# Optimization experiments

Measured on AMD Instinct MI355X. Metric: run time of the kernel, lower is better.

The kernel has to match this reference:

```python
import jax, jax.numpy as jnp
import numpy as np

B, N, E = 4, 4096, 65536
FIN, FOUT = 128, 64
ALPHA = 0.2          # LeakyReLU negative slope
NEG = -9e15          # mask value from original code


def setup_inputs() -> dict:
    key = jax.random.key(0)
    k1, k2, k3, k4 = jax.random.split(key, 4)
    h = jax.random.normal(k1, (B, N, FIN), dtype=jnp.float32)
    edge_index = jax.random.randint(k2, (B, 2, E), 0, N, dtype=jnp.int32)
    # Xavier-uniform-like params
    W = jax.random.uniform(k3, (FIN, FOUT), jnp.float32, -1.0, 1.0) * (1.414 * np.sqrt(6.0 / (FIN + FOUT)))
    a = jax.random.uniform(k4, (2 * FOUT, 1), jnp.float32, -1.0, 1.0) * (1.414 * np.sqrt(6.0 / (2 * FOUT + 1)))
    return {"h": h, "edge_index": edge_index, "W": W, "a": a}


def reference(h, edge_index, W, a):
    # Wh: [B, N, FOUT]
    Wh = jnp.einsum('bnf,fo->bno', h, W)
    Wh_flat = Wh.reshape(-1, FOUT)  # [B*N, FOUT]

    # Faithful to original: raw node ids (< N) index the flattened tensor,
    # i.e. edge features are gathered from batch 0's rows.
    src = edge_index[:, 0].reshape(-1)  # [B*E]
    tgt = edge_index[:, 1].reshape(-1)  # [B*E]
    a_input = jnp.concatenate([Wh_flat[src], Wh_flat[tgt]], axis=1)  # [B*E, 2*FOUT]
    e = (a_input @ a)[:, 0]  # [B*E]

    b_idx = jnp.repeat(jnp.arange(B), E)
    e_dense = jnp.zeros((B, N, N), e.dtype).at[b_idx, src, tgt].set(e)
    e_dense = jax.nn.leaky_relu(e_dense, ALPHA)

    attention = jnp.where(e_dense > 0, e_dense, NEG)
    attention = jax.nn.softmax(attention, axis=1)  # softmax over dim=1 as in original
    # dropout p=0.0 -> no-op

    h_prime = jnp.einsum('bmn,bnf->bmf', attention, Wh)  # [B, N, FOUT]
    return jax.nn.elu(h_prime)  # concat=True path
```

## Files before the change

kernel.cpp:

```cpp
#include <hip/hip_runtime.h>
#include <hip/hip_bf16.h>

#define BB 4
#define NN 4096
#define EE 65536
#define FIN 128
#define FOUT 64
#define CAP 64

__global__ __launch_bounds__(256) void phase0_kernel(
        const float* __restrict__ h, const float* __restrict__ W, const float* __restrict__ a,
        float* __restrict__ Wh, int* __restrict__ deg, float* __restrict__ D,
        unsigned* __restrict__ bitmap, float* __restrict__ as_, float* __restrict__ at_,
        float* __restrict__ base) {
    __shared__ union {
        struct { float hs[32][132]; float Ws[64][64]; } wh;
        float Wa[256];
    } smem;
    int tid = threadIdx.x;
    int bid = blockIdx.x;
    if (bid < 512) {
        long row0 = (long)bid * 32;
        for (int i = tid; i < 1024; i += 256) {
            float4 v = ((const float4*)(h + row0 * FIN))[i];
            int r = (i * 4) >> 7, c = (i * 4) & 127;
            *(float4*)&smem.wh.hs[r][c] = v;
        }
        int tx = tid & 15, ty = tid >> 4;
        int c0 = tx * 4, r0 = ty * 2;
        float acc[2][4] = {};
        for (int kk = 0; kk < 128; kk += 64) {
            __syncthreads();
            for (int i = tid; i < 1024; i += 256) {
                float4 v = ((const float4*)(W + kk * FOUT))[i];
                int k = (i * 4) >> 6, c = (i * 4) & 63;
                *(float4*)&smem.wh.Ws[k][c] = v;
            }
            __syncthreads();
#pragma unroll
            for (int k = 0; k < 64; k += 4) {
                float4 w0 = *(const float4*)&smem.wh.Ws[k][c0];
                float4 w1 = *(const float4*)&smem.wh.Ws[k + 1][c0];
                float4 w2 = *(const float4*)&smem.wh.Ws[k + 2][c0];
                float4 w3 = *(const float4*)&smem.wh.Ws[k + 3][c0];
#pragma unroll
                for (int r = 0; r < 2; ++r) {
                    float4 hv = *(const float4*)&smem.wh.hs[r0 + r][kk + k];
                    acc[r][0] += hv.x * w0.x + hv.y * w1.x + hv.z * w2.x + hv.w * w3.x;
                    acc[r][1] += hv.x * w0.y + hv.y * w1.y + hv.z * w2.y + hv.w * w3.y;
                    acc[r][2] += hv.x * w0.z + hv.y * w1.z + hv.z * w2.z + hv.w * w3.z;
                    acc[r][3] += hv.x * w0.w + hv.y * w1.w + hv.z * w2.w + hv.w * w3.w;
                }
            }
        }
#pragma unroll
        for (int r = 0; r < 2; ++r)
            *(float4*)&Wh[(row0 + r0 + r) * FOUT + c0] = *(float4*)&acc[r][0];
    } else {
        int local = bid - 512;
        uint4* bm4 = (uint4*)(bitmap + (long)local * 4096);
        for (int i = tid; i < 1024; i += 256) bm4[i] = make_uint4(0u, 0u, 0u, 0u);
        int gid2 = local * 256 + tid;
        if (gid2 < BB * NN) { deg[gid2] = 0; D[gid2] = 0.f; }
        if (gid2 < BB * FOUT) base[gid2] = 0.f;
        {
            int half = tid >> 7, k = tid & 127;
            const float* wr = W + k * FOUT;
            const float* av = a + half * FOUT;
            float s = 0.f;
#pragma unroll
            for (int f2 = 0; f2 < FOUT; ++f2) s += wr[f2] * av[f2];
            smem.Wa[half * 128 + k] = s;
        }
        __syncthreads();
        int lane = tid & 63, wv = tid >> 6;
#pragma unroll
        for (int r = 0; r < 2; ++r) {
            int n = local * 8 + wv * 2 + r;
            float h0v = h[(long)n * FIN + lane];
            float h1v = h[(long)n * FIN + 64 + lane];
            float ps = h0v * smem.Wa[lane] + h1v * smem.Wa[64 + lane];
            float pt = h0v * smem.Wa[128 + lane] + h1v * smem.Wa[192 + lane];
            for (int off = 32; off; off >>= 1) {
                ps += __shfl_down(ps, off);
                pt += __shfl_down(pt, off);
            }
            if (lane == 0) { as_[n] = ps; at_[n] = pt; }
        }
    }
}

__global__ void edge_kernel(const int* __restrict__ ei, const float* __restrict__ as_,
                            const float* __restrict__ at_, unsigned* __restrict__ bitmap,
                            int* __restrict__ deg, int* __restrict__ csr,
                            float* __restrict__ D) {
    int idx = blockIdx.x * 256 + threadIdx.x;
    int b = idx >> 16;
    int j = idx & 65535;
    const int* eb = ei + (long)b * 2 * EE;
    int s = eb[j], t = eb[EE + j];
    float as_s = as_[s];
    if (as_s + at_[t] > 0.f) {
        int row = (b << 12) | s;
        long bit = ((long)row << 12) | t;
        unsigned m = 1u << (bit & 31);
        unsigned old = atomicOr(&bitmap[bit >> 5], m);
        if (!(old & m)) {
            atomicAdd(&D[(b << 12) | t], expf(as_s));
            int slot = atomicAdd(&deg[row], 1);
            if (slot < CAP) csr[row * CAP + slot] = t;
        }
    }
}

__global__ __launch_bounds__(256) void base_kernel(
        const float* __restrict__ D, const float* __restrict__ Wh,
        float* __restrict__ base) {
    __shared__ float part[4][64];
    int tid = threadIdx.x, lane = tid & 63, wv = tid >> 6;
    int bid = blockIdx.x;
    int b = bid >> 4, chunk = bid & 15;
    const float* Db = D + (b << 12);
    const float* Whb = Wh + (((long)b << 12) * FOUT);
    int t0 = chunk * 256 + wv * 64;
    float dv = Db[t0 + lane];
    unsigned long long zmask = __ballot(dv == 0.f);
    float bacc = 0.f;
    while (zmask) {
        int k = __ffsll(zmask) - 1;
        zmask &= zmask - 1;
        bacc += Whb[(t0 + k) * FOUT + lane];
    }
    part[wv][lane] = bacc;
    __syncthreads();
    if (wv == 0) {
        float s = part[0][lane] + part[1][lane] + part[2][lane] + part[3][lane];
        atomicAdd(&base[(b << 6) | lane], s * (1.0f / NN));
    }
}

__global__ __launch_bounds__(256) void gather_kernel(
        const int* __restrict__ deg, const int* __restrict__ csr,
        const float* __restrict__ as_, const float* __restrict__ D,
        const float* __restrict__ Wh, const float* __restrict__ base,
        float* __restrict__ out) {
    int tid = threadIdx.x;
    int lane = tid & 63, wv = tid >> 6;
    int bid = blockIdx.x;
    int b = bid >> 8;
    const float* Db = D + (b << 12);
    const float* Whb = Wh + (((long)b << 12) * FOUT);
    float bsv = base[(b << 6) | lane];

    int row0 = bid * 16 + wv * 4;
    int d0 = min(deg[row0], CAP), d1 = min(deg[row0 + 1], CAP);
    int d2 = min(deg[row0 + 2], CAP), d3 = min(deg[row0 + 3], CAP);
    float E0 = expf(as_[row0 & 4095]), E1 = expf(as_[(row0 + 1) & 4095]);
    float E2 = expf(as_[(row0 + 2) & 4095]), E3 = expf(as_[(row0 + 3) & 4095]);
    const int* c0p = csr + (long)row0 * CAP;
    const int* c1p = c0p + CAP;
    const int* c2p = c1p + CAP;
    const int* c3p = c2p + CAP;
    float a0 = 0.f, a1 = 0.f, a2 = 0.f, a3 = 0.f;
    int dmax = max(max(d0, d1), max(d2, d3));
    for (int j = 0; j < dmax; ++j) {
        if (j < d0) { int t = c0p[j]; a0 += (E0 / Db[t]) * Whb[t * FOUT + lane]; }
        if (j < d1) { int t = c1p[j]; a1 += (E1 / Db[t]) * Whb[t * FOUT + lane]; }
        if (j < d2) { int t = c2p[j]; a2 += (E2 / Db[t]) * Whb[t * FOUT + lane]; }
        if (j < d3) { int t = c3p[j]; a3 += (E3 / Db[t]) * Whb[t * FOUT + lane]; }
    }
    float x0 = a0 + bsv, x1 = a1 + bsv, x2 = a2 + bsv, x3 = a3 + bsv;
    out[(long)row0 * FOUT + lane] = x0 > 0.f ? x0 : expm1f(x0);
    out[(long)(row0 + 1) * FOUT + lane] = x1 > 0.f ? x1 : expm1f(x1);
    out[(long)(row0 + 2) * FOUT + lane] = x2 > 0.f ? x2 : expm1f(x2);
    out[(long)(row0 + 3) * FOUT + lane] = x3 > 0.f ? x3 : expm1f(x3);
}

extern "C" void kernel_launch(void* const* d_in, const int* in_sizes, int n_in,
                              void* d_out, int out_size, void* d_ws, size_t ws_size,
                              hipStream_t stream) {
    const float* h  = (const float*)d_in[0];
    const int*   ei = (const int*)d_in[1];
    const float* W  = (const float*)d_in[2];
    const float* a  = (const float*)d_in[3];
    float* out = (float*)d_out;

    char* ws = (char*)d_ws;
    float*    Wh     = (float*)(ws);
    int*      csr    = (int*)(ws + 4194304);
    unsigned* bitmap = (unsigned*)(ws + 8388608);
    int*      deg    = (int*)(ws + 16777216);
    float*    D      = (float*)(ws + 16842752);
    float*    as_    = (float*)(ws + 16908288);
    float*    at_    = (float*)(ws + 16924672);
    float*    base   = (float*)(ws + 16941056);

    phase0_kernel<<<1024, 256, 0, stream>>>(h, W, a, Wh, deg, D, bitmap, as_, at_, base);
    edge_kernel<<<(BB * EE) / 256, 256, 0, stream>>>(ei, as_, at_, bitmap, deg, csr, D);
    base_kernel<<<64, 256, 0, stream>>>(D, Wh, base);
    gather_kernel<<<(BB * NN) / 16, 256, 0, stream>>>(deg, csr, as_, D, Wh, base, out);
}
```

Before: 95.19 us.

## Fuse four kernels into three, overlapping edge build with GEMM and base with gather

Moves the bitmap/deg/D initialization and the as/at projections into a dedicated init kernel. The edge scatter is merged into the Wh GEMM kernel so both run in one launch. The base reduction is merged into the gather kernel: 64 blocks compute base and signal a device-scope counter, while gather blocks spin-wait on that counter before the final add. This removes a kernel launch boundary and lets base and gather overlap, at the cost of a spin-wait that relies on the base blocks being scheduled, bounded only by a guard count.

```diff
diff --git a/kernel.cpp b/kernel.cpp
--- a/kernel.cpp
+++ b/kernel.cpp
@@ -8,23 +8,79 @@
 #define FOUT 64
 #define CAP 64
 
-__global__ __launch_bounds__(256) void phase0_kernel(
+__global__ __launch_bounds__(256) void init_kernel(
         const float* __restrict__ h, const float* __restrict__ W, const float* __restrict__ a,
-        float* __restrict__ Wh, int* __restrict__ deg, float* __restrict__ D,
-        unsigned* __restrict__ bitmap, float* __restrict__ as_, float* __restrict__ at_,
-        float* __restrict__ base) {
-    __shared__ union {
-        struct { float hs[32][132]; float Ws[64][64]; } wh;
-        float Wa[256];
-    } smem;
-    int tid = threadIdx.x;
-    int bid = blockIdx.x;
+        unsigned* __restrict__ bitmap, int* __restrict__ deg, float* __restrict__ D,
+        float* __restrict__ base, unsigned* __restrict__ done,
+        float* __restrict__ as_, float* __restrict__ at_) {
+    __shared__ float Wa[256];
+    int tid = threadIdx.x, bid = blockIdx.x;
+    uint4* bm4 = (uint4*)(bitmap + (long)bid * 4096);
+    for (int i = tid; i < 1024; i += 256) bm4[i] = make_uint4(0u, 0u, 0u, 0u);
+    int gid = bid * 256 + tid;
+    if (gid < BB * NN) { deg[gid] = 0; D[gid] = 0.f; }
+    if (gid < BB * FOUT) base[gid] = 0.f;
+    if (gid == 0) *done = 0u;
+    {
+        int half = tid >> 7, k = tid & 127;
+        const float* wr = W + k * FOUT;
+        const float* av = a + half * FOUT;
+        float s = 0.f;
+#pragma unroll
+        for (int f2 = 0; f2 < FOUT; ++f2) s += wr[f2] * av[f2];
+        Wa[half * 128 + k] = s;
+    }
+    __syncthreads();
+    int lane = tid & 63, wv = tid >> 6;
+#pragma unroll
+    for (int r = 0; r < 2; ++r) {
+        int n = bid * 8 + wv * 2 + r;
+        float h0v = h[(long)n * FIN + lane];
+        float h1v = h[(long)n * FIN + 64 + lane];
+        float ps = h0v * Wa[lane] + h1v * Wa[64 + lane];
+        float pt = h0v * Wa[128 + lane] + h1v * Wa[192 + lane];
+        for (int off = 32; off; off >>= 1) {
+            ps += __shfl_down(ps, off);
+            pt += __shfl_down(pt, off);
+        }
+        if (lane == 0) { as_[n] = ps; at_[n] = pt; }
+    }
+}
+
+__global__ __launch_bounds__(256) void edge_gemm_kernel(
+        const float* __restrict__ h, const int* __restrict__ ei,
+        const float* __restrict__ W, const float* __restrict__ as_,
+        const float* __restrict__ at_, unsigned* __restrict__ bitmap,
+        int* __restrict__ deg, int* __restrict__ csr, float* __restrict__ D,
+        float* __restrict__ Wh) {
+    __shared__ struct { float hs[32][132]; float Ws[64][64]; } smem;
+    int tid = threadIdx.x, bid = blockIdx.x;
+
+    {
+        int idx = bid * 256 + tid;
+        int b = idx >> 16, j = idx & 65535;
+        const int* eb = ei + (long)b * 2 * EE;
+        int s = eb[j], t = eb[EE + j];
+        float as_s = as_[s];
+        if (as_s + at_[t] > 0.f) {
+            int row = (b << 12) | s;
+            long bit = ((long)row << 12) | t;
+            unsigned m = 1u << (bit & 31);
+            unsigned old = atomicOr(&bitmap[bit >> 5], m);
+            if (!(old & m)) {
+                atomicAdd(&D[(b << 12) | t], expf(as_s));
+                int slot = atomicAdd(&deg[row], 1);
+                if (slot < CAP) csr[row * CAP + slot] = t;
+            }
+        }
+    }
+
     if (bid < 512) {
         long row0 = (long)bid * 32;
         for (int i = tid; i < 1024; i += 256) {
             float4 v = ((const float4*)(h + row0 * FIN))[i];
             int r = (i * 4) >> 7, c = (i * 4) & 127;
-            *(float4*)&smem.wh.hs[r][c] = v;
+            *(float4*)&smem.hs[r][c] = v;
         }
         int tx = tid & 15, ty = tid >> 4;
         int c0 = tx * 4, r0 = ty * 2;
@@ -34,18 +90,18 @@
             for (int i = tid; i < 1024; i += 256) {
                 float4 v = ((const float4*)(W + kk * FOUT))[i];
                 int k = (i * 4) >> 6, c = (i * 4) & 63;
-                *(float4*)&smem.wh.Ws[k][c] = v;
+                *(float4*)&smem.Ws[k][c] = v;
             }
             __syncthreads();
 #pragma unroll
             for (int k = 0; k < 64; k += 4) {
-                float4 w0 = *(const float4*)&smem.wh.Ws[k][c0];
-                float4 w1 = *(const float4*)&smem.wh.Ws[k + 1][c0];
-                float4 w2 = *(const float4*)&smem.wh.Ws[k + 2][c0];
-                float4 w3 = *(const float4*)&smem.wh.Ws[k + 3][c0];
+                float4 w0 = *(const float4*)&smem.Ws[k][c0];
+                float4 w1 = *(const float4*)&smem.Ws[k + 1][c0];
+                float4 w2 = *(const float4*)&smem.Ws[k + 2][c0];
+                float4 w3 = *(const float4*)&smem.Ws[k + 3][c0];
 #pragma unroll
                 for (int r = 0; r < 2; ++r) {
-                    float4 hv = *(const float4*)&smem.wh.hs[r0 + r][kk + k];
+                    float4 hv = *(const float4*)&smem.hs[r0 + r][kk + k];
                     acc[r][0] += hv.x * w0.x + hv.y * w1.x + hv.z * w2.x + hv.w * w3.x;
                     acc[r][1] += hv.x * w0.y + hv.y * w1.y + hv.z * w2.y + hv.w * w3.y;
                     acc[r][2] += hv.x * w0.z + hv.y * w1.z + hv.z * w2.z + hv.w * w3.z;
@@ -56,103 +112,49 @@
 #pragma unroll
         for (int r = 0; r < 2; ++r)
             *(float4*)&Wh[(row0 + r0 + r) * FOUT + c0] = *(float4*)&acc[r][0];
-    } else {
-        int local = bid - 512;
-        uint4* bm4 = (uint4*)(bitmap + (long)local * 4096);
-        for (int i = tid; i < 1024; i += 256) bm4[i] = make_uint4(0u, 0u, 0u, 0u);
-        int gid2 = local * 256 + tid;
-        if (gid2 < BB * NN) { deg[gid2] = 0; D[gid2] = 0.f; }
-        if (gid2 < BB * FOUT) base[gid2] = 0.f;
-        {
-            int half = tid >> 7, k = tid & 127;
-            const float* wr = W + k * FOUT;
-            const float* av = a + half * FOUT;
-            float s = 0.f;
-#pragma unroll
-            for (int f2 = 0; f2 < FOUT; ++f2) s += wr[f2] * av[f2];
-            smem.Wa[half * 128 + k] = s;
-        }
-        __syncthreads();
-        int lane = tid & 63, wv = tid >> 6;
-#pragma unroll
-        for (int r = 0; r < 2; ++r) {
-            int n = local * 8 + wv * 2 + r;
-            float h0v = h[(long)n * FIN + lane];
-            float h1v = h[(long)n * FIN + 64 + lane];
-            float ps = h0v * smem.Wa[lane] + h1v * smem.Wa[64 + lane];
-            float pt = h0v * smem.Wa[128 + lane] + h1v * smem.Wa[192 + lane];
-            for (int off = 32; off; off >>= 1) {
-                ps += __shfl_down(ps, off);
-                pt += __shfl_down(pt, off);
-            }
-            if (lane == 0) { as_[n] = ps; at_[n] = pt; }
-        }
-    }
-}
-
-__global__ void edge_kernel(const int* __restrict__ ei, const float* __restrict__ as_,
-                            const float* __restrict__ at_, unsigned* __restrict__ bitmap,
-                            int* __restrict__ deg, int* __restrict__ csr,
-                            float* __restrict__ D) {
-    int idx = blockIdx.x * 256 + threadIdx.x;
-    int b = idx >> 16;
-    int j = idx & 65535;
-    const int* eb = ei + (long)b * 2 * EE;
-    int s = eb[j], t = eb[EE + j];
-    float as_s = as_[s];
-    if (as_s + at_[t] > 0.f) {
-        int row = (b << 12) | s;
-        long bit = ((long)row << 12) | t;
-        unsigned m = 1u << (bit & 31);
-        unsigned old = atomicOr(&bitmap[bit >> 5], m);
-        if (!(old & m)) {
-            atomicAdd(&D[(b << 12) | t], expf(as_s));
-            int slot = atomicAdd(&deg[row], 1);
-            if (slot < CAP) csr[row * CAP + slot] = t;
-        }
-    }
-}
-
-__global__ __launch_bounds__(256) void base_kernel(
-        const float* __restrict__ D, const float* __restrict__ Wh,
-        float* __restrict__ base) {
+    }
+}
+
+__global__ __launch_bounds__(256) void base_gather_kernel(
+        const int* __restrict__ deg, const int* __restrict__ csr,
+        const float* __restrict__ as_, const float* __restrict__ D,
+        const float* __restrict__ Wh, float* __restrict__ base,
+        unsigned* __restrict__ done, float* __restrict__ out) {
     __shared__ float part[4][64];
     int tid = threadIdx.x, lane = tid & 63, wv = tid >> 6;
     int bid = blockIdx.x;
-    int b = bid >> 4, chunk = bid & 15;
+
+    if (bid < 64) {
+        int b = bid >> 4, chunk = bid & 15;
+        const float* Db = D + (b << 12);
+        const float* Whb = Wh + (((long)b << 12) * FOUT);
+        int t0 = chunk * 256 + wv * 64;
+        float dv = Db[t0 + lane];
+        unsigned long long zmask = __ballot(dv == 0.f);
+        float bacc = 0.f;
+        while (zmask) {
+            int k = __ffsll(zmask) - 1;
+            zmask &= zmask - 1;
+            bacc += Whb[(t0 + k) * FOUT + lane];
+        }
+        part[wv][lane] = bacc;
+        __syncthreads();
+        if (wv == 0) {
+            float s = part[0][lane] + part[1][lane] + part[2][lane] + part[3][lane];
+            atomicAdd(&base[(b << 6) | lane], s * (1.0f / NN));
+        }
+        __syncthreads();
+        if (tid == 0)
+            __hip_atomic_fetch_add(done, 1u, __ATOMIC_RELEASE, __HIP_MEMORY_SCOPE_AGENT);
+        return;
+    }
+
+    int gid = bid - 64;
+    int b = gid >> 8;
     const float* Db = D + (b << 12);
     const float* Whb = Wh + (((long)b << 12) * FOUT);
-    int t0 = chunk * 256 + wv * 64;
-    float dv = Db[t0 + lane];
-    unsigned long long zmask = __ballot(dv == 0.f);
-    float bacc = 0.f;
-    while (zmask) {
-        int k = __ffsll(zmask) - 1;
-        zmask &= zmask - 1;
-        bacc += Whb[(t0 + k) * FOUT + lane];
-    }
-    part[wv][lane] = bacc;
-    __syncthreads();
-    if (wv == 0) {
-        float s = part[0][lane] + part[1][lane] + part[2][lane] + part[3][lane];
-        atomicAdd(&base[(b << 6) | lane], s * (1.0f / NN));
-    }
-}
-
-__global__ __launch_bounds__(256) void gather_kernel(
-        const int* __restrict__ deg, const int* __restrict__ csr,
-        const float* __restrict__ as_, const float* __restrict__ D,
-        const float* __restrict__ Wh, const float* __restrict__ base,
-        float* __restrict__ out) {
-    int tid = threadIdx.x;
-    int lane = tid & 63, wv = tid >> 6;
-    int bid = blockIdx.x;
-    int b = bid >> 8;
-    const float* Db = D + (b << 12);
-    const float* Whb = Wh + (((long)b << 12) * FOUT);
-    float bsv = base[(b << 6) | lane];
-
-    int row0 = bid * 16 + wv * 4;
+
+    int row0 = gid * 16 + wv * 4;
     int d0 = min(deg[row0], CAP), d1 = min(deg[row0 + 1], CAP);
     int d2 = min(deg[row0 + 2], CAP), d3 = min(deg[row0 + 3], CAP);
     float E0 = expf(as_[row0 & 4095]), E1 = expf(as_[(row0 + 1) & 4095]);
@@ -169,6 +171,17 @@
         if (j < d2) { int t = c2p[j]; a2 += (E2 / Db[t]) * Whb[t * FOUT + lane]; }
         if (j < d3) { int t = c3p[j]; a3 += (E3 / Db[t]) * Whb[t * FOUT + lane]; }
     }
+
+    if (tid == 0) {
+        int guard = 0;
+        while (__hip_atomic_load(done, __ATOMIC_ACQUIRE, __HIP_MEMORY_SCOPE_AGENT) < 64u &&
+               ++guard < (1 << 22))
+            __builtin_amdgcn_s_sleep(2);
+    }
+    __syncthreads();
+    float bsv = __hip_atomic_load(&base[(b << 6) | lane], __ATOMIC_ACQUIRE,
+                                  __HIP_MEMORY_SCOPE_AGENT);
+
     float x0 = a0 + bsv, x1 = a1 + bsv, x2 = a2 + bsv, x3 = a3 + bsv;
     out[(long)row0 * FOUT + lane] = x0 > 0.f ? x0 : expm1f(x0);
     out[(long)(row0 + 1) * FOUT + lane] = x1 > 0.f ? x1 : expm1f(x1);
@@ -194,9 +207,9 @@
     float*    as_    = (float*)(ws + 16908288);
     float*    at_    = (float*)(ws + 16924672);
     float*    base   = (float*)(ws + 16941056);
-
-    phase0_kernel<<<1024, 256, 0, stream>>>(h, W, a, Wh, deg, D, bitmap, as_, at_, base);
-    edge_kernel<<<(BB * EE) / 256, 256, 0, stream>>>(ei, as_, at_, bitmap, deg, csr, D);
-    base_kernel<<<64, 256, 0, stream>>>(D, Wh, base);
-    gather_kernel<<<(BB * NN) / 16, 256, 0, stream>>>(deg, csr, as_, D, Wh, base, out);
-}
+    unsigned* done   = (unsigned*)(ws + 16942080);
+
+    init_kernel<<<512, 256, 0, stream>>>(h, W, a, bitmap, deg, D, base, done, as_, at_);
+    edge_gemm_kernel<<<1024, 256, 0, stream>>>(h, ei, W, as_, at_, bitmap, deg, csr, D, Wh);
+    base_gather_kernel<<<1088, 256, 0, stream>>>(deg, csr, as_, D, Wh, base, done, out);
+}
```

Result: slower. 116.7 us (+22.6%).

## Fuse base and gather kernels using an atomic completion counter

Applied to the files above, without the earlier changes.

Merges base_kernel into the gather kernel. The first 64 blocks compute the base term and increment a global done counter with release semantics. Gather blocks do their neighbour accumulation first, then spin on the counter before reading base. The gather is also restructured to one row per wave: neighbour indices and weights are loaded lane-parallel and broadcast with shuffles, with 8 loads batched at a time. This removes a kernel launch boundary and improves memory-level parallelism. It relies on the base blocks being scheduled first to avoid a long spin, and the guard bounds the wait.

```diff
diff --git a/kernel.cpp b/kernel.cpp
--- a/kernel.cpp
+++ b/kernel.cpp
@@ -12,7 +12,7 @@
         const float* __restrict__ h, const float* __restrict__ W, const float* __restrict__ a,
         float* __restrict__ Wh, int* __restrict__ deg, float* __restrict__ D,
         unsigned* __restrict__ bitmap, float* __restrict__ as_, float* __restrict__ at_,
-        float* __restrict__ base) {
+        float* __restrict__ base, unsigned* __restrict__ done) {
     __shared__ union {
         struct { float hs[32][132]; float Ws[64][64]; } wh;
         float Wa[256];
@@ -63,6 +63,7 @@
         int gid2 = local * 256 + tid;
         if (gid2 < BB * NN) { deg[gid2] = 0; D[gid2] = 0.f; }
         if (gid2 < BB * FOUT) base[gid2] = 0.f;
+        if (gid2 == 0) *done = 0u;
         {
             int half = tid >> 7, k = tid & 127;
             const float* wr = W + k * FOUT;
@@ -113,67 +114,81 @@
     }
 }
 
-__global__ __launch_bounds__(256) void base_kernel(
-        const float* __restrict__ D, const float* __restrict__ Wh,
-        float* __restrict__ base) {
+__global__ __launch_bounds__(256) void base_gather_kernel(
+        const int* __restrict__ deg, const int* __restrict__ csr,
+        const float* __restrict__ as_, const float* __restrict__ D,
+        const float* __restrict__ Wh, float* __restrict__ base,
+        unsigned* __restrict__ done, float* __restrict__ out) {
     __shared__ float part[4][64];
     int tid = threadIdx.x, lane = tid & 63, wv = tid >> 6;
     int bid = blockIdx.x;
-    int b = bid >> 4, chunk = bid & 15;
+
+    if (bid < 64) {
+        int b = bid >> 4, chunk = bid & 15;
+        const float* Db = D + (b << 12);
+        const float* Whb = Wh + (((long)b << 12) * FOUT);
+        int t0 = chunk * 256 + wv * 64;
+        float dv = Db[t0 + lane];
+        unsigned long long zmask = __ballot(dv == 0.f);
+        float bacc = 0.f;
+        while (zmask) {
+            int k = __ffsll(zmask) - 1;
+            zmask &= zmask - 1;
+            bacc += Whb[(t0 + k) * FOUT + lane];
+        }
+        part[wv][lane] = bacc;
+        __syncthreads();
+        if (wv == 0) {
+            float s = part[0][lane] + part[1][lane] + part[2][lane] + part[3][lane];
+            atomicAdd(&base[(b << 6) | lane], s * (1.0f / NN));
+        }
+        __syncthreads();
+        if (tid == 0)
+            __hip_atomic_fetch_add(done, 1u, __ATOMIC_RELEASE, __HIP_MEMORY_SCOPE_AGENT);
+        return;
+    }
+
+    int row = (bid - 64) * 4 + wv;
+    int b = row >> 12;
     const float* Db = D + (b << 12);
     const float* Whb = Wh + (((long)b << 12) * FOUT);
-    int t0 = chunk * 256 + wv * 64;
-    float dv = Db[t0 + lane];
-    unsigned long long zmask = __ballot(dv == 0.f);
-    float bacc = 0.f;
-    while (zmask) {
-        int k = __ffsll(zmask) - 1;
-        zmask &= zmask - 1;
-        bacc += Whb[(t0 + k) * FOUT + lane];
-    }
-    part[wv][lane] = bacc;
+    int d = min(deg[row], CAP);
+    float E = expf(as_[row & 4095]);
+
+    int t = 0;
+    float w = 0.f;
+    if (lane < d) {
+        t = csr[(long)row * CAP + lane];
+        w = E / Db[t];
+    }
+
+    float acc = 0.f;
+    for (int j0 = 0; j0 < d; j0 += 8) {
+        int tt[8];
+        float ww[8], vv[8];
+#pragma unroll
+        for (int k = 0; k < 8; ++k) {
+            tt[k] = __shfl(t, j0 + k);
+            ww[k] = __shfl(w, j0 + k);
+        }
+#pragma unroll
+        for (int k = 0; k < 8; ++k) vv[k] = Whb[tt[k] * FOUT + lane];
+#pragma unroll
+        for (int k = 0; k < 8; ++k) acc += ww[k] * vv[k];
+    }
+
+    if (tid == 0) {
+        int guard = 0;
+        while (__hip_atomic_load(done, __ATOMIC_ACQUIRE, __HIP_MEMORY_SCOPE_AGENT) < 64u &&
+               ++guard < (1 << 22))
+            __builtin_amdgcn_s_sleep(2);
+    }
     __syncthreads();
-    if (wv == 0) {
-        float s = part[0][lane] + part[1][lane] + part[2][lane] + part[3][lane];
-        atomicAdd(&base[(b << 6) | lane], s * (1.0f / NN));
-    }
-}
-
-__global__ __launch_bounds__(256) void gather_kernel(
-        const int* __restrict__ deg, const int* __restrict__ csr,
-        const float* __restrict__ as_, const float* __restrict__ D,
-        const float* __restrict__ Wh, const float* __restrict__ base,
-        float* __restrict__ out) {
-    int tid = threadIdx.x;
-    int lane = tid & 63, wv = tid >> 6;
-    int bid = blockIdx.x;
-    int b = bid >> 8;
-    const float* Db = D + (b << 12);
-    const float* Whb = Wh + (((long)b << 12) * FOUT);
-    float bsv = base[(b << 6) | lane];
-
-    int row0 = bid * 16 + wv * 4;
-    int d0 = min(deg[row0], CAP), d1 = min(deg[row0 + 1], CAP);
-    int d2 = min(deg[row0 + 2], CAP), d3 = min(deg[row0 + 3], CAP);
-    float E0 = expf(as_[row0 & 4095]), E1 = expf(as_[(row0 + 1) & 4095]);
-    float E2 = expf(as_[(row0 + 2) & 4095]), E3 = expf(as_[(row0 + 3) & 4095]);
-    const int* c0p = csr + (long)row0 * CAP;
-    const int* c1p = c0p + CAP;
-    const int* c2p = c1p + CAP;
-    const int* c3p = c2p + CAP;
-    float a0 = 0.f, a1 = 0.f, a2 = 0.f, a3 = 0.f;
-    int dmax = max(max(d0, d1), max(d2, d3));
-    for (int j = 0; j < dmax; ++j) {
-        if (j < d0) { int t = c0p[j]; a0 += (E0 / Db[t]) * Whb[t * FOUT + lane]; }
-        if (j < d1) { int t = c1p[j]; a1 += (E1 / Db[t]) * Whb[t * FOUT + lane]; }
-        if (j < d2) { int t = c2p[j]; a2 += (E2 / Db[t]) * Whb[t * FOUT + lane]; }
-        if (j < d3) { int t = c3p[j]; a3 += (E3 / Db[t]) * Whb[t * FOUT + lane]; }
-    }
-    float x0 = a0 + bsv, x1 = a1 + bsv, x2 = a2 + bsv, x3 = a3 + bsv;
-    out[(long)row0 * FOUT + lane] = x0 > 0.f ? x0 : expm1f(x0);
-    out[(long)(row0 + 1) * FOUT + lane] = x1 > 0.f ? x1 : expm1f(x1);
-    out[(long)(row0 + 2) * FOUT + lane] = x2 > 0.f ? x2 : expm1f(x2);
-    out[(long)(row0 + 3) * FOUT + lane] = x3 > 0.f ? x3 : expm1f(x3);
+    float bsv = __hip_atomic_load(&base[(b << 6) | lane], __ATOMIC_ACQUIRE,
+                                  __HIP_MEMORY_SCOPE_AGENT);
+
+    float x = acc + bsv;
+    out[(long)row * FOUT + lane] = x > 0.f ? x : expm1f(x);
 }
 
 extern "C" void kernel_launch(void* const* d_in, const int* in_sizes, int n_in,
@@ -194,9 +209,11 @@
     float*    as_    = (float*)(ws + 16908288);
     float*    at_    = (float*)(ws + 16924672);
     float*    base   = (float*)(ws + 16941056);
-
-    phase0_kernel<<<1024, 256, 0, stream>>>(h, W, a, Wh, deg, D, bitmap, as_, at_, base);
+    unsigned* done   = (unsigned*)(ws + 16942080);
+
+    phase0_kernel<<<1024, 256, 0, stream>>>(h, W, a, Wh, deg, D, bitmap, as_, at_,
+                                            base, done);
     edge_kernel<<<(BB * EE) / 256, 256, 0, stream>>>(ei, as_, at_, bitmap, deg, csr, D);
-    base_kernel<<<64, 256, 0, stream>>>(D, Wh, base);
-    gather_kernel<<<(BB * NN) / 16, 256, 0, stream>>>(deg, csr, as_, D, Wh, base, out);
-}
+    base_gather_kernel<<<64 + (BB * NN) / 4, 256, 0, stream>>>(deg, csr, as_, D, Wh,
+                                                               base, done, out);
+}
```

New measurement: 257.7 us. 2.71x slower.
